# Performance work log

Hardware: AMD Instinct MI355X
Metric: run time of the kernel (lower is better)

The kernel has to match this reference:

```python
import jax, jax.numpy as jnp
import numpy as np

B = 65536
CH = 12          # chans
L = 63           # length
FBAND = 14
ZDIM = 2
FLEN = 7         # adaptive filter taps
PAD = 3          # (FLEN-1)//2
VLEN = L - FLEN + 1   # 57, 'same'-conv then crop == valid conv
FG_H = 35
EN1, EN2 = 16, 32
KW, ST = 6, 3
EN_OUT = EN2 * 5      # 160
DE_H = ZDIM * 5       # 10
DE_OUT = 50
BN_EPS = 1e-5


def setup_inputs() -> dict:
    key = jax.random.key(0)
    ks = jax.random.split(key, 24)
    f32 = jnp.float32

    def rn(k, shape, scale=0.1):
        return jax.random.normal(k, shape, f32) * scale

    return {
        "raw_eeg": jax.random.normal(ks[0], (B, CH, L), f32),
        "eegf": jax.random.normal(ks[1], (B, CH * FBAND), f32),
        "eps": jax.random.normal(ks[2], (B, ZDIM), f32),
        # filter generator: Linear(168->35), Tanh, Linear(35->7), Tanh
        "fg_w1": rn(ks[3], (FG_H, CH * FBAND)), "fg_b1": rn(ks[4], (FG_H,)),
        "fg_w2": rn(ks[5], (FLEN, FG_H)), "fg_b2": rn(ks[6], (FLEN,)),
        # encoder convs + batchnorms
        "enc_w1": rn(ks[7], (EN1, CH, KW)), "enc_b1": rn(ks[8], (EN1,)),
        "bn1_g": jnp.ones((EN1,), f32), "bn1_b": jnp.zeros((EN1,), f32),
        "enc_w2": rn(ks[9], (EN2, EN1, KW)), "enc_b2": rn(ks[10], (EN2,)),
        "bn2_g": jnp.ones((EN2,), f32), "bn2_b": jnp.zeros((EN2,), f32),
        # latent heads
        "mu_w": rn(ks[11], (ZDIM, EN_OUT)), "mu_b": rn(ks[12], (ZDIM,)),
        "lv_w": rn(ks[13], (ZDIM, EN_OUT)), "lv_b": rn(ks[14], (ZDIM,)),
        # decoder: Linear(2->10), Tanh, Linear(10->50), Tanh
        "de_w1": rn(ks[15], (DE_H, ZDIM)), "de_b1": rn(ks[16], (DE_H,)),
        "de_w2": rn(ks[17], (DE_OUT, DE_H)), "de_b2": rn(ks[18], (DE_OUT,)),
    }


def _linear(x, w, b):
    return x @ w.T + b


def _batchnorm(x, g, b):
    # torch BatchNorm1d, training mode: biased variance over (N, L) per channel
    mean = jnp.mean(x, axis=(0, 2), keepdims=True)
    var = jnp.mean(jnp.square(x - mean), axis=(0, 2), keepdims=True)
    xn = (x - mean) * jax.lax.rsqrt(var + BN_EPS)
    return xn * g[None, :, None] + b[None, :, None]


def _conv1d(x, w, b, stride):
    y = jax.lax.conv_general_dilated(
        x, w, window_strides=(stride,), padding="VALID",
        dimension_numbers=("NCH", "OIH", "NCH"))
    return y + b[None, :, None]


def reference(raw_eeg, eegf, eps,
              fg_w1, fg_b1, fg_w2, fg_b2,
              enc_w1, enc_b1, bn1_g, bn1_b,
              enc_w2, enc_b2, bn2_g, bn2_b,
              mu_w, mu_b, lv_w, lv_b,
              de_w1, de_b1, de_w2, de_b2):
    bsz = raw_eeg.shape[0]
    # per-sample 7-tap adaptive filter  [B, FLEN]
    filt = jnp.tanh(_linear(jnp.tanh(_linear(eegf, fg_w1, fg_b1)), fg_w2, fg_b2))
    # per-sample depthwise cross-correlation, 'same' conv then pad:-pad crop
    # == VALID correlation: eeg[b,c,t] = sum_k raw[b,c,t+k] * filt[b,k]
    eeg = sum(raw_eeg[:, :, k:k + VLEN] * filt[:, None, k, None]
              for k in range(FLEN))                      # [B, CH, 57]
    # encoder
    h = jnp.tanh(_batchnorm(_conv1d(eeg, enc_w1, enc_b1, ST), bn1_g, bn1_b))   # [B,16,18]
    h = jnp.tanh(_batchnorm(_conv1d(h, enc_w2, enc_b2, ST), bn2_g, bn2_b))     # [B,32,5]
    h = h.reshape(bsz, -1)                                # [B,160]
    mu = _linear(h, mu_w, mu_b)                           # [B,2]
    logvar = _linear(h, lv_w, lv_b)                       # [B,2]
    z = mu + eps * jnp.exp(0.5 * logvar)                  # reparameterize
    d = jnp.tanh(_linear(z, de_w1, de_b1))
    output = jnp.tanh(_linear(d, de_w2, de_b2))           # [B,50]
    return (output, mu, logvar)
```

## Files before the change

### kernel.cpp

```cpp
#include <hip/hip_runtime.h>
#include <hip/hip_bf16.h>

#define BATCH   65536
#define NCHAN   12
#define LRAW    63
#define CHF     168
#define FLEN    7
#define VLEN    57
#define FGH     35
#define EN1     16
#define EN2     32
#define KWID    6
#define LC1     18
#define LC2     5

#define SH1     64
#define SH2     32

static const size_t WS_STATS1 = 0;
static const size_t WS_STATS2 = 2048;
static const size_t WS_COEF   = 4096;
static const size_t WS_W1T    = 4192;
static const size_t WS_W2T    = WS_W1T + 1152;
static const size_t WS_FILT   = WS_W2T + 3072;
static const size_t WS_C1     = WS_FILT + (size_t)BATCH * 8;

__global__ void k_init(const float* __restrict__ ew1, const float* __restrict__ ew2,
                       float* __restrict__ w1t, float* __restrict__ w2t,
                       float* __restrict__ stats) {
    int t = threadIdx.x;
    for (int i = t; i < 4096; i += 256) stats[i] = 0.f;
    for (int i = t; i < EN1 * NCHAN * KWID; i += 256) {
        int oc = i / (NCHAN * KWID); int r = i % (NCHAN * KWID);
        w1t[r * EN1 + oc] = ew1[i];
    }
    for (int i = t; i < EN2 * EN1 * KWID; i += 256) {
        int oc = i / (EN1 * KWID); int r = i % (EN1 * KWID);
        w2t[r * EN2 + oc] = ew2[i];
    }
}

__global__ __launch_bounds__(256) void k_fg(
        const float* __restrict__ eegf,
        const float* __restrict__ w1, const float* __restrict__ b1,
        const float* __restrict__ w2, const float* __restrict__ b2,
        float* __restrict__ filt) {
    int b = blockIdx.x * 256 + threadIdx.x;
    const float* xr = eegf + (size_t)b * CHF;
    float acc[FGH];
#pragma unroll
    for (int j = 0; j < FGH; j++) acc[j] = b1[j];
#pragma unroll 1
    for (int t0 = 0; t0 < CHF; t0 += 56) {
        float x[56];
#pragma unroll
        for (int q = 0; q < 14; q++) {
            float4 v = *reinterpret_cast<const float4*>(xr + t0 + 4 * q);
            x[4*q] = v.x; x[4*q+1] = v.y; x[4*q+2] = v.z; x[4*q+3] = v.w;
        }
#pragma unroll 1
        for (int j = 0; j < FGH; j++) {
            const float* wr = w1 + (size_t)j * CHF + t0;
            float s0 = 0.f, s1 = 0.f, s2 = 0.f, s3 = 0.f;
#pragma unroll
            for (int q = 0; q < 14; q++) {
                s0 = fmaf(x[4*q],   wr[4*q],   s0);
                s1 = fmaf(x[4*q+1], wr[4*q+1], s1);
                s2 = fmaf(x[4*q+2], wr[4*q+2], s2);
                s3 = fmaf(x[4*q+3], wr[4*q+3], s3);
            }
            acc[j] += (s0 + s1) + (s2 + s3);
        }
    }
    float fa[FLEN];
#pragma unroll
    for (int k = 0; k < FLEN; k++) fa[k] = b2[k];
#pragma unroll 1
    for (int j = 0; j < FGH; j++) {
        float h = tanhf(acc[j]);
#pragma unroll
        for (int k = 0; k < FLEN; k++) fa[k] = fmaf(h, w2[k * FGH + j], fa[k]);
    }
    float4 o0, o1;
    o0.x = tanhf(fa[0]); o0.y = tanhf(fa[1]); o0.z = tanhf(fa[2]); o0.w = tanhf(fa[3]);
    o1.x = tanhf(fa[4]); o1.y = tanhf(fa[5]); o1.z = tanhf(fa[6]); o1.w = 0.f;
    float4* fo = reinterpret_cast<float4*>(filt + (size_t)b * 8);
    fo[0] = o0; fo[1] = o1;
}

__global__ __launch_bounds__(320) void k_conv1(
        const float* __restrict__ raw, const float* __restrict__ encb1,
        const float* __restrict__ filtbuf, const float* __restrict__ w1t,
        float* __restrict__ c1, float* __restrict__ stats1) {
    __shared__ float4 rawt4[3024];
    __shared__ float filts[16][9];
    float* rawt = (float*)rawt4;
    const int tid = threadIdx.x;
    const int s0b = blockIdx.x * 16;
    const float4* src4 = reinterpret_cast<const float4*>(raw + (size_t)s0b * 756);
#pragma unroll
    for (int k = 0; k < 10; k++) {
        int idx = tid + k * 320;
        if (idx < 3024) rawt4[idx] = src4[idx];
    }
    if (tid < 112) {
        int s = tid / 7, k = tid % 7;
        filts[s][k] = filtbuf[(size_t)(s0b + s) * 8 + k];
    }
    __syncthreads();
    const int s = tid & 15;
    const int pg = tid >> 4;
    float acc[EN1];
#pragma unroll
    for (int o = 0; o < EN1; o++) acc[o] = encb1[o];
    if (pg < 18) {
        const float f0 = filts[s][0], f1 = filts[s][1], f2 = filts[s][2], f3 = filts[s][3],
                    f4 = filts[s][4], f5 = filts[s][5], f6 = filts[s][6];
        const float* rbase = rawt + s * 756 + 3 * pg;
#pragma unroll 1
        for (int c = 0; c < NCHAN; c++) {
            const float* rp = rbase + c * 63;
            float rv[12];
#pragma unroll
            for (int j = 0; j < 12; j++) rv[j] = rp[j];
            float e[KWID];
#pragma unroll
            for (int j = 0; j < KWID; j++) {
                float v = f0 * rv[j];
                v = fmaf(f1, rv[j+1], v);
                v = fmaf(f2, rv[j+2], v);
                v = fmaf(f3, rv[j+3], v);
                v = fmaf(f4, rv[j+4], v);
                v = fmaf(f5, rv[j+5], v);
                v = fmaf(f6, rv[j+6], v);
                e[j] = v;
            }
            const float* wp = w1t + c * (KWID * EN1);
#pragma unroll
            for (int j = 0; j < KWID; j++)
#pragma unroll
                for (int o = 0; o < EN1; o++)
                    acc[o] = fmaf(e[j], wp[j * EN1 + o], acc[o]);
        }
    }
    __syncthreads();
    float* c1t = rawt;
    if (pg < 18) {
#pragma unroll
        for (int o = 0; o < EN1; o++) c1t[s * 305 + o * 19 + pg] = acc[o];
    }
    __syncthreads();
    float* c1g = c1 + (size_t)s0b * 288;
#pragma unroll 1
    for (int ss = 0; ss < 16; ss++) {
        if (tid < 288) {
            int oc = tid / 18, p = tid - oc * 18;
            c1g[ss * 288 + tid] = c1t[ss * 305 + oc * 19 + p];
        }
    }
    if (tid < 256) {
        const int oc = tid >> 4, g = tid & 15;
        float sm = 0.f, sq = 0.f;
#pragma unroll
        for (int p = 0; p < 18; p++) {
            float v = c1t[g * 305 + oc * 19 + p];
            sm += v; sq = fmaf(v, v, sq);
        }
#pragma unroll
        for (int m = 8; m >= 1; m >>= 1) {
            sm += __shfl_xor(sm, m);
            sq += __shfl_xor(sq, m);
        }
        if (g == 0) {
            float* base = stats1 + (blockIdx.x & (SH1 - 1)) * 32;
            atomicAdd(base + oc, sm);
            atomicAdd(base + 16 + oc, sq);
        }
    }
}

__global__ void k_bnfin(const float* __restrict__ g, const float* __restrict__ bb,
                        const float* __restrict__ shards, int nsh, int nch,
                        float* __restrict__ ca, float* __restrict__ cb,
                        float invn) {
    int t = threadIdx.x;
    if (t < nch) {
        float sm = 0.f, sq = 0.f;
        for (int i = 0; i < nsh; i++) {
            sm += shards[i * 2 * nch + t];
            sq += shards[i * 2 * nch + nch + t];
        }
        float mean = sm * invn;
        float var  = sq * invn - mean * mean;
        float a = g[t] * rsqrtf(var + 1e-5f);
        ca[t] = a;
        cb[t] = bb[t] - mean * a;
    }
}

__global__ __launch_bounds__(256) void k_conv2(
        const float* __restrict__ encb2, const float* __restrict__ bn1c,
        const float* __restrict__ w2t, float* __restrict__ c1,
        float* __restrict__ stats2) {
    __shared__ float e1s[32 * 289];
    const int tid = threadIdx.x;
    const int s0b = blockIdx.x * 32;
    float* c1g = c1 + (size_t)s0b * 288;
    const int sl = tid >> 3, g = tid & 7;
    {
        const float4* row4 = reinterpret_cast<const float4*>(c1g + sl * 288);
#pragma unroll 1
        for (int kk = 0; kk < 9; kk++) {
            int fo = kk * 8 + g;
            float4 v = row4[fo];
            float r[4] = {v.x, v.y, v.z, v.w};
            int i0 = fo * 4;
#pragma unroll
            for (int u = 0; u < 4; u++) {
                int i = i0 + u;
                int ch = i / 18;
                e1s[sl * 289 + i] = tanhf(fmaf(r[u], bn1c[ch], bn1c[16 + ch]));
            }
        }
    }
    __syncthreads();
    const int s = tid & 31, p = tid >> 5;
    float acc[EN2];
#pragma unroll
    for (int o = 0; o < EN2; o++) acc[o] = encb2[o];
    if (p < 5) {
        const float* eS = e1s + s * 289;
#pragma unroll 1
        for (int c = 0; c < EN1; c++) {
#pragma unroll
            for (int j = 0; j < KWID; j++) {
                float ev = eS[c * 18 + 3 * p + j];
                const float* wp = w2t + (c * KWID + j) * EN2;
#pragma unroll
                for (int o = 0; o < EN2; o++) acc[o] = fmaf(ev, wp[o], acc[o]);
            }
        }
    }
    __syncthreads();
    float* c2t = e1s;
    if (p < 5) {
#pragma unroll
        for (int o = 0; o < EN2; o++) c2t[s * 161 + o * 5 + p] = acc[o];
    }
    __syncthreads();
    {
        float4* row4 = reinterpret_cast<float4*>(c1g + sl * 288);
#pragma unroll 1
        for (int kk = 0; kk < 5; kk++) {
            int fo = kk * 8 + g;
            int i0 = fo * 4;
            float4 w;
            w.x = c2t[sl * 161 + i0];
            w.y = c2t[sl * 161 + i0 + 1];
            w.z = c2t[sl * 161 + i0 + 2];
            w.w = c2t[sl * 161 + i0 + 3];
            row4[fo] = w;
        }
    }
    {
        const int oc = tid >> 3, g8 = tid & 7;
        float sm = 0.f, sq = 0.f;
#pragma unroll 1
        for (int mm = 0; mm < 4; mm++) {
            int ss = g8 + 8 * mm;
#pragma unroll
            for (int pp = 0; pp < 5; pp++) {
                float v = c2t[ss * 161 + oc * 5 + pp];
                sm += v; sq = fmaf(v, v, sq);
            }
        }
#pragma unroll
        for (int m = 4; m >= 1; m >>= 1) {
            sm += __shfl_xor(sm, m);
            sq += __shfl_xor(sq, m);
        }
        if (g8 == 0) {
            float* base = stats2 + (blockIdx.x & (SH2 - 1)) * 64;
            atomicAdd(base + oc, sm);
            atomicAdd(base + 32 + oc, sq);
        }
    }
}

__global__ __launch_bounds__(256) void k_head(
        const float* __restrict__ eps,
        const float* __restrict__ muw, const float* __restrict__ mub,
        const float* __restrict__ lvw, const float* __restrict__ lvb,
        const float* __restrict__ dw1, const float* __restrict__ db1,
        const float* __restrict__ dw2, const float* __restrict__ db2,
        const float* __restrict__ c2, const float* __restrict__ bn2c,
        float* __restrict__ out) {
    int gid = blockIdx.x * 256 + threadIdx.x;
    int b = gid >> 2, q = gid & 3;
    const float4* c2v = reinterpret_cast<const float4*>(c2 + (size_t)b * 288 + q * 40);
    float m0 = 0.f, m1 = 0.f, l0 = 0.f, l1 = 0.f;
#pragma unroll 1
    for (int t = 0; t < 10; t++) {
        float4 v = c2v[t];
        float r[4] = {v.x, v.y, v.z, v.w};
#pragma unroll
        for (int u = 0; u < 4; u++) {
            int idx = q * 40 + t * 4 + u;
            int ch = idx / 5;
            float h = tanhf(fmaf(r[u], bn2c[ch], bn2c[32 + ch]));
            m0 = fmaf(h, muw[idx],       m0);
            m1 = fmaf(h, muw[160 + idx], m1);
            l0 = fmaf(h, lvw[idx],       l0);
            l1 = fmaf(h, lvw[160 + idx], l1);
        }
    }
#pragma unroll
    for (int m = 1; m <= 2; m <<= 1) {
        m0 += __shfl_xor(m0, m); m1 += __shfl_xor(m1, m);
        l0 += __shfl_xor(l0, m); l1 += __shfl_xor(l1, m);
    }
    m0 += mub[0]; m1 += mub[1]; l0 += lvb[0]; l1 += lvb[1];
    float2 ev = *reinterpret_cast<const float2*>(eps + (size_t)b * 2);
    float z0 = fmaf(ev.x, expf(0.5f * l0), m0);
    float z1 = fmaf(ev.y, expf(0.5f * l1), m1);
    float d[10];
#pragma unroll
    for (int j = 0; j < 10; j++)
        d[j] = tanhf(fmaf(z1, dw1[j * 2 + 1], fmaf(z0, dw1[j * 2], db1[j])));
    float* orow = out + (size_t)b * 50;
    int nkk = (q == 3) ? 7 : 6;
#pragma unroll 1
    for (int kk = 0; kk < nkk; kk++) {
        int o = (q * 6 + kk) * 2;
        float s0 = db2[o], s1 = db2[o + 1];
#pragma unroll
        for (int j = 0; j < 10; j++) {
            s0 = fmaf(d[j], dw2[o * 10 + j],       s0);
            s1 = fmaf(d[j], dw2[(o + 1) * 10 + j], s1);
        }
        float2 w; w.x = tanhf(s0); w.y = tanhf(s1);
        *reinterpret_cast<float2*>(orow + o) = w;
    }
    if (q == 0)
        *reinterpret_cast<float2*>(out + (size_t)BATCH * 50 + (size_t)b * 2) = make_float2(m0, m1);
    if (q == 1)
        *reinterpret_cast<float2*>(out + (size_t)BATCH * 52 + (size_t)b * 2) = make_float2(l0, l1);
}

extern "C" void kernel_launch(void* const* d_in, const int* in_sizes, int n_in,
                              void* d_out, int out_size, void* d_ws, size_t ws_size,
                              hipStream_t stream) {
    (void)in_sizes; (void)n_in; (void)out_size; (void)ws_size;
    const float* raw  = (const float*)d_in[0];
    const float* eegf = (const float*)d_in[1];
    const float* eps  = (const float*)d_in[2];
    const float* fgw1 = (const float*)d_in[3];
    const float* fgb1 = (const float*)d_in[4];
    const float* fgw2 = (const float*)d_in[5];
    const float* fgb2 = (const float*)d_in[6];
    const float* ew1  = (const float*)d_in[7];
    const float* eb1  = (const float*)d_in[8];
    const float* bn1g = (const float*)d_in[9];
    const float* bn1b = (const float*)d_in[10];
    const float* ew2  = (const float*)d_in[11];
    const float* eb2  = (const float*)d_in[12];
    const float* bn2g = (const float*)d_in[13];
    const float* bn2b = (const float*)d_in[14];
    const float* muw  = (const float*)d_in[15];
    const float* mub  = (const float*)d_in[16];
    const float* lvw  = (const float*)d_in[17];
    const float* lvb  = (const float*)d_in[18];
    const float* dw1  = (const float*)d_in[19];
    const float* db1  = (const float*)d_in[20];
    const float* dw2  = (const float*)d_in[21];
    const float* db2  = (const float*)d_in[22];

    float* ws     = (float*)d_ws;
    float* stats1 = ws + WS_STATS1;
    float* stats2 = ws + WS_STATS2;
    float* coef   = ws + WS_COEF;
    float* w1t    = ws + WS_W1T;
    float* w2t    = ws + WS_W2T;
    float* filt   = ws + WS_FILT;
    float* c1     = ws + WS_C1;
    float* out    = (float*)d_out;

    hipLaunchKernelGGL(k_init, dim3(1), dim3(256), 0, stream, ew1, ew2, w1t, w2t, stats1);
    hipLaunchKernelGGL(k_fg, dim3(256), dim3(256), 0, stream, eegf, fgw1, fgb1, fgw2, fgb2, filt);
    hipLaunchKernelGGL(k_conv1, dim3(4096), dim3(320), 0, stream, raw, eb1, filt, w1t, c1, stats1);
    hipLaunchKernelGGL(k_bnfin, dim3(1), dim3(64), 0, stream,
                       bn1g, bn1b, stats1, SH1, 16, coef, coef + 16,
                       1.0f / ((float)BATCH * (float)LC1));
    hipLaunchKernelGGL(k_conv2, dim3(2048), dim3(256), 0, stream, eb2, coef, w2t, c1, stats2);
    hipLaunchKernelGGL(k_bnfin, dim3(1), dim3(64), 0, stream,
                       bn2g, bn2b, stats2, SH2, 32, coef + 32, coef + 64,
                       1.0f / ((float)BATCH * (float)LC2));
    hipLaunchKernelGGL(k_head, dim3(1024), dim3(256), 0, stream,
                       eps, muw, mub, lvw, lvb, dw1, db1, dw2, db2, c1, coef + 32, out);
}
```

Measured before the change: 629.9 us.

## Store conv intermediates as bf16, fuse BN finalize, fast tanh, double-buffer conv1

```diff
diff --git a/kernel.cpp b/kernel.cpp
--- a/kernel.cpp
+++ b/kernel.cpp
@@ -6,7 +6,6 @@
 #define LRAW    63
 #define CHF     168
 #define FLEN    7
-#define VLEN    57
 #define FGH     35
 #define EN1     16
 #define EN2     32
@@ -19,11 +18,23 @@
 
 static const size_t WS_STATS1 = 0;
 static const size_t WS_STATS2 = 2048;
-static const size_t WS_COEF   = 4096;
-static const size_t WS_W1T    = 4192;
+static const size_t WS_W1T    = 4096;
 static const size_t WS_W2T    = WS_W1T + 1152;
 static const size_t WS_FILT   = WS_W2T + 3072;
 static const size_t WS_C1     = WS_FILT + (size_t)BATCH * 8;
+static const size_t WS_C2     = WS_C1 + (size_t)18 * BATCH * 16 / 2;
+
+__device__ __forceinline__ float ftanh(float x) {
+    float e = __expf(2.0f * x);
+    return fmaf(-2.0f, __builtin_amdgcn_rcpf(e + 1.0f), 1.0f);
+}
+__device__ __forceinline__ unsigned int bfr(float x) {
+    unsigned int u = __float_as_uint(x);
+    return (u + 0x7fffu + ((u >> 16) & 1u)) >> 16;
+}
+__device__ __forceinline__ float bf2f(unsigned int us) {
+    return __uint_as_float(us << 16);
+}
 
 __global__ void k_init(const float* __restrict__ ew1, const float* __restrict__ ew2,
                        float* __restrict__ w1t, float* __restrict__ w2t,
@@ -58,7 +69,7 @@
             float4 v = *reinterpret_cast<const float4*>(xr + t0 + 4 * q);
             x[4*q] = v.x; x[4*q+1] = v.y; x[4*q+2] = v.z; x[4*q+3] = v.w;
         }
-#pragma unroll 1
+#pragma unroll 5
         for (int j = 0; j < FGH; j++) {
             const float* wr = w1 + (size_t)j * CHF + t0;
             float s0 = 0.f, s1 = 0.f, s2 = 0.f, s3 = 0.f;
@@ -77,13 +88,13 @@
     for (int k = 0; k < FLEN; k++) fa[k] = b2[k];
 #pragma unroll 1
     for (int j = 0; j < FGH; j++) {
-        float h = tanhf(acc[j]);
+        float h = ftanh(acc[j]);
 #pragma unroll
         for (int k = 0; k < FLEN; k++) fa[k] = fmaf(h, w2[k * FGH + j], fa[k]);
     }
     float4 o0, o1;
-    o0.x = tanhf(fa[0]); o0.y = tanhf(fa[1]); o0.z = tanhf(fa[2]); o0.w = tanhf(fa[3]);
-    o1.x = tanhf(fa[4]); o1.y = tanhf(fa[5]); o1.z = tanhf(fa[6]); o1.w = 0.f;
+    o0.x = ftanh(fa[0]); o0.y = ftanh(fa[1]); o0.z = ftanh(fa[2]); o0.w = ftanh(fa[3]);
+    o1.x = ftanh(fa[4]); o1.y = ftanh(fa[5]); o1.z = ftanh(fa[6]); o1.w = 0.f;
     float4* fo = reinterpret_cast<float4*>(filt + (size_t)b * 8);
     fo[0] = o0; fo[1] = o1;
 }
@@ -91,144 +102,166 @@
 __global__ __launch_bounds__(320) void k_conv1(
         const float* __restrict__ raw, const float* __restrict__ encb1,
         const float* __restrict__ filtbuf, const float* __restrict__ w1t,
-        float* __restrict__ c1, float* __restrict__ stats1) {
+        unsigned short* __restrict__ c1, float* __restrict__ stats1) {
     __shared__ float4 rawt4[3024];
-    __shared__ float filts[16][9];
+    __shared__ float filts[2][16][8];
+    __shared__ float part[5][32];
     float* rawt = (float*)rawt4;
     const int tid = threadIdx.x;
-    const int s0b = blockIdx.x * 16;
+    const int s0b = blockIdx.x * 32;
     const float4* src4 = reinterpret_cast<const float4*>(raw + (size_t)s0b * 756);
 #pragma unroll
     for (int k = 0; k < 10; k++) {
         int idx = tid + k * 320;
         if (idx < 3024) rawt4[idx] = src4[idx];
     }
-    if (tid < 112) {
-        int s = tid / 7, k = tid % 7;
-        filts[s][k] = filtbuf[(size_t)(s0b + s) * 8 + k];
+    if (tid < 256) {
+        int tl = tid >> 7, r = tid & 127, s = r >> 3, k = r & 7;
+        filts[tl][s][k] = filtbuf[(size_t)(s0b + tl * 16 + s) * 8 + k];
     }
     __syncthreads();
+    float4 rr[10];
+#pragma unroll
+    for (int k = 0; k < 10; k++) {
+        int idx = tid + k * 320;
+        if (idx < 3024) rr[k] = src4[3024 + idx];
+    }
     const int s = tid & 15;
     const int pg = tid >> 4;
-    float acc[EN1];
-#pragma unroll
-    for (int o = 0; o < EN1; o++) acc[o] = encb1[o];
-    if (pg < 18) {
-        const float f0 = filts[s][0], f1 = filts[s][1], f2 = filts[s][2], f3 = filts[s][3],
-                    f4 = filts[s][4], f5 = filts[s][5], f6 = filts[s][6];
-        const float* rbase = rawt + s * 756 + 3 * pg;
-#pragma unroll 1
-        for (int c = 0; c < NCHAN; c++) {
-            const float* rp = rbase + c * 63;
-            float rv[12];
-#pragma unroll
-            for (int j = 0; j < 12; j++) rv[j] = rp[j];
-            float e[KWID];
-#pragma unroll
-            for (int j = 0; j < KWID; j++) {
-                float v = f0 * rv[j];
-                v = fmaf(f1, rv[j+1], v);
-                v = fmaf(f2, rv[j+2], v);
-                v = fmaf(f3, rv[j+3], v);
-                v = fmaf(f4, rv[j+4], v);
-                v = fmaf(f5, rv[j+5], v);
-                v = fmaf(f6, rv[j+6], v);
-                e[j] = v;
-            }
-            const float* wp = w1t + c * (KWID * EN1);
-#pragma unroll
-            for (int j = 0; j < KWID; j++)
-#pragma unroll
-                for (int o = 0; o < EN1; o++)
-                    acc[o] = fmaf(e[j], wp[j * EN1 + o], acc[o]);
-        }
-    }
-    __syncthreads();
-    float* c1t = rawt;
-    if (pg < 18) {
-#pragma unroll
-        for (int o = 0; o < EN1; o++) c1t[s * 305 + o * 19 + pg] = acc[o];
-    }
-    __syncthreads();
-    float* c1g = c1 + (size_t)s0b * 288;
-#pragma unroll 1
-    for (int ss = 0; ss < 16; ss++) {
-        if (tid < 288) {
-            int oc = tid / 18, p = tid - oc * 18;
-            c1g[ss * 288 + tid] = c1t[ss * 305 + oc * 19 + p];
-        }
-    }
-    if (tid < 256) {
-        const int oc = tid >> 4, g = tid & 15;
-        float sm = 0.f, sq = 0.f;
-#pragma unroll
-        for (int p = 0; p < 18; p++) {
-            float v = c1t[g * 305 + oc * 19 + p];
-            sm += v; sq = fmaf(v, v, sq);
-        }
-#pragma unroll
-        for (int m = 8; m >= 1; m >>= 1) {
-            sm += __shfl_xor(sm, m);
-            sq += __shfl_xor(sq, m);
-        }
-        if (g == 0) {
-            float* base = stats1 + (blockIdx.x & (SH1 - 1)) * 32;
-            atomicAdd(base + oc, sm);
-            atomicAdd(base + 16 + oc, sq);
-        }
-    }
-}
-
-__global__ void k_bnfin(const float* __restrict__ g, const float* __restrict__ bb,
-                        const float* __restrict__ shards, int nsh, int nch,
-                        float* __restrict__ ca, float* __restrict__ cb,
-                        float invn) {
-    int t = threadIdx.x;
-    if (t < nch) {
-        float sm = 0.f, sq = 0.f;
-        for (int i = 0; i < nsh; i++) {
-            sm += shards[i * 2 * nch + t];
-            sq += shards[i * 2 * nch + nch + t];
-        }
-        float mean = sm * invn;
-        float var  = sq * invn - mean * mean;
-        float a = g[t] * rsqrtf(var + 1e-5f);
-        ca[t] = a;
-        cb[t] = bb[t] - mean * a;
+    const int wv = tid >> 6;
+#pragma unroll 1
+    for (int tl = 0; tl < 2; tl++) {
+        float acc[EN1];
+        if (pg < 18) {
+#pragma unroll
+            for (int o = 0; o < EN1; o++) acc[o] = encb1[o];
+            const float f0 = filts[tl][s][0], f1 = filts[tl][s][1], f2 = filts[tl][s][2],
+                        f3 = filts[tl][s][3], f4 = filts[tl][s][4], f5 = filts[tl][s][5],
+                        f6 = filts[tl][s][6];
+            const float* rbase = rawt + s * 756 + 3 * pg;
+#pragma unroll 1
+            for (int c = 0; c < NCHAN; c++) {
+                const float* rp = rbase + c * 63;
+                float rv[12];
+#pragma unroll
+                for (int j = 0; j < 12; j++) rv[j] = rp[j];
+                float e[KWID];
+#pragma unroll
+                for (int j = 0; j < KWID; j++) {
+                    float v = f0 * rv[j];
+                    v = fmaf(f1, rv[j+1], v);
+                    v = fmaf(f2, rv[j+2], v);
+                    v = fmaf(f3, rv[j+3], v);
+                    v = fmaf(f4, rv[j+4], v);
+                    v = fmaf(f5, rv[j+5], v);
+                    v = fmaf(f6, rv[j+6], v);
+                    e[j] = v;
+                }
+                const float* wp = w1t + c * (KWID * EN1);
+#pragma unroll
+                for (int j = 0; j < KWID; j++)
+#pragma unroll
+                    for (int o = 0; o < EN1; o++)
+                        acc[o] = fmaf(e[j], wp[j * EN1 + o], acc[o]);
+            }
+            unsigned int w[8];
+#pragma unroll
+            for (int o = 0; o < 8; o++)
+                w[o] = bfr(acc[2*o]) | (bfr(acc[2*o+1]) << 16);
+            size_t base = ((size_t)pg * BATCH + (size_t)(s0b + tl*16 + s)) * 16;
+            uint4* dst = reinterpret_cast<uint4*>(c1 + base);
+            dst[0] = make_uint4(w[0], w[1], w[2], w[3]);
+            dst[1] = make_uint4(w[4], w[5], w[6], w[7]);
+        } else {
+#pragma unroll
+            for (int o = 0; o < EN1; o++) acc[o] = 0.f;
+        }
+        float sq[EN1];
+#pragma unroll
+        for (int o = 0; o < EN1; o++) sq[o] = acc[o] * acc[o];
+#pragma unroll
+        for (int m = 1; m < 64; m <<= 1) {
+#pragma unroll
+            for (int o = 0; o < EN1; o++) {
+                acc[o] += __shfl_xor(acc[o], m);
+                sq[o]  += __shfl_xor(sq[o], m);
+            }
+        }
+        if ((tid & 63) == 0) {
+#pragma unroll
+            for (int o = 0; o < EN1; o++) {
+                part[wv][o]      = acc[o];
+                part[wv][16 + o] = sq[o];
+            }
+        }
+        __syncthreads();
+        if (tid < 32) {
+            float v = part[0][tid] + part[1][tid] + part[2][tid] + part[3][tid] + part[4][tid];
+            atomicAdd(stats1 + (blockIdx.x & (SH1 - 1)) * 32 + tid, v);
+        }
+        if (tl == 0) {
+#pragma unroll
+            for (int k = 0; k < 10; k++) {
+                int idx = tid + k * 320;
+                if (idx < 3024) rawt4[idx] = rr[k];
+            }
+            __syncthreads();
+        }
     }
 }
 
 __global__ __launch_bounds__(256) void k_conv2(
-        const float* __restrict__ encb2, const float* __restrict__ bn1c,
-        const float* __restrict__ w2t, float* __restrict__ c1,
+        const float* __restrict__ encb2,
+        const float* __restrict__ bn1g, const float* __restrict__ bn1b,
+        const float* __restrict__ stats1, const float* __restrict__ w2t,
+        const unsigned short* __restrict__ c1, unsigned short* __restrict__ c2,
         float* __restrict__ stats2) {
     __shared__ float e1s[32 * 289];
+    __shared__ float bn1c[32];
+    __shared__ float part[4][64];
     const int tid = threadIdx.x;
     const int s0b = blockIdx.x * 32;
-    float* c1g = c1 + (size_t)s0b * 288;
-    const int sl = tid >> 3, g = tid & 7;
-    {
-        const float4* row4 = reinterpret_cast<const float4*>(c1g + sl * 288);
-#pragma unroll 1
-        for (int kk = 0; kk < 9; kk++) {
-            int fo = kk * 8 + g;
-            float4 v = row4[fo];
-            float r[4] = {v.x, v.y, v.z, v.w};
-            int i0 = fo * 4;
+    if (tid < 16) {
+        float sm = 0.f, sqr = 0.f;
+#pragma unroll 8
+        for (int i = 0; i < SH1; i++) {
+            sm  += stats1[i * 32 + tid];
+            sqr += stats1[i * 32 + 16 + tid];
+        }
+        const float invn = 1.0f / ((float)BATCH * (float)LC1);
+        float mean = sm * invn;
+        float var  = sqr * invn - mean * mean;
+        float a = bn1g[tid] * rsqrtf(var + 1e-5f);
+        bn1c[tid] = a;
+        bn1c[16 + tid] = bn1b[tid] - mean * a;
+    }
+    __syncthreads();
+    const uint4* c1u = reinterpret_cast<const uint4*>(c1);
+#pragma unroll
+    for (int k = 0; k < 5; k++) {
+        int idx = tid + k * 256;
+        if (idx < 1152) {
+            int p = idx >> 6, rem = idx & 63, ss = rem >> 1, half = rem & 1;
+            uint4 v = c1u[((size_t)p * BATCH + (s0b + ss)) * 2 + half];
+            unsigned int ww[4] = {v.x, v.y, v.z, v.w};
+            float* eb = e1s + ss * 289 + p;
 #pragma unroll
             for (int u = 0; u < 4; u++) {
-                int i = i0 + u;
-                int ch = i / 18;
-                e1s[sl * 289 + i] = tanhf(fmaf(r[u], bn1c[ch], bn1c[16 + ch]));
+                int oc0 = half * 8 + 2 * u;
+                float f0 = bf2f(ww[u] & 0xffffu);
+                float f1 = __uint_as_float(ww[u] & 0xffff0000u);
+                eb[oc0 * 18]       = ftanh(fmaf(f0, bn1c[oc0],     bn1c[16 + oc0]));
+                eb[(oc0 + 1) * 18] = ftanh(fmaf(f1, bn1c[oc0 + 1], bn1c[16 + oc0 + 1]));
             }
         }
     }
     __syncthreads();
     const int s = tid & 31, p = tid >> 5;
+    const bool act = (p < 5);
     float acc[EN2];
-#pragma unroll
-    for (int o = 0; o < EN2; o++) acc[o] = encb2[o];
-    if (p < 5) {
+    if (act) {
+#pragma unroll
+        for (int o = 0; o < EN2; o++) acc[o] = encb2[o];
         const float* eS = e1s + s * 289;
 #pragma unroll 1
         for (int c = 0; c < EN1; c++) {
@@ -240,50 +273,37 @@
                 for (int o = 0; o < EN2; o++) acc[o] = fmaf(ev, wp[o], acc[o]);
             }
         }
+#pragma unroll
+        for (int o = 0; o < EN2; o++)
+            c2[(size_t)(o * 5 + p) * BATCH + (s0b + s)] = (unsigned short)bfr(acc[o]);
+    } else {
+#pragma unroll
+        for (int o = 0; o < EN2; o++) acc[o] = 0.f;
+    }
+    float sq[EN2];
+#pragma unroll
+    for (int o = 0; o < EN2; o++) sq[o] = acc[o] * acc[o];
+#pragma unroll
+    for (int m = 1; m < 64; m <<= 1) {
+#pragma unroll
+        for (int o = 0; o < EN2; o++) {
+            acc[o] += __shfl_xor(acc[o], m);
+            sq[o]  += __shfl_xor(sq[o], m);
+        }
+    }
+    const int lane = tid & 63, wv = tid >> 6;
+    if (lane == 0) {
+#pragma unroll
+        for (int o = 0; o < EN2; o++) part[wv][o] = acc[o];
+    }
+    if (lane == 1) {
+#pragma unroll
+        for (int o = 0; o < EN2; o++) part[wv][32 + o] = sq[o];
     }
     __syncthreads();
-    float* c2t = e1s;
-    if (p < 5) {
-#pragma unroll
-        for (int o = 0; o < EN2; o++) c2t[s * 161 + o * 5 + p] = acc[o];
-    }
-    __syncthreads();
-    {
-        float4* row4 = reinterpret_cast<float4*>(c1g + sl * 288);
-#pragma unroll 1
-        for (int kk = 0; kk < 5; kk++) {
-            int fo = kk * 8 + g;
-            int i0 = fo * 4;
-            float4 w;
-            w.x = c2t[sl * 161 + i0];
-            w.y = c2t[sl * 161 + i0 + 1];
-            w.z = c2t[sl * 161 + i0 + 2];
-            w.w = c2t[sl * 161 + i0 + 3];
-            row4[fo] = w;
-        }
-    }
-    {
-        const int oc = tid >> 3, g8 = tid & 7;
-        float sm = 0.f, sq = 0.f;
-#pragma unroll 1
-        for (int mm = 0; mm < 4; mm++) {
-            int ss = g8 + 8 * mm;
-#pragma unroll
-            for (int pp = 0; pp < 5; pp++) {
-                float v = c2t[ss * 161 + oc * 5 + pp];
-                sm += v; sq = fmaf(v, v, sq);
-            }
-        }
-#pragma unroll
-        for (int m = 4; m >= 1; m >>= 1) {
-            sm += __shfl_xor(sm, m);
-            sq += __shfl_xor(sq, m);
-        }
-        if (g8 == 0) {
-            float* base = stats2 + (blockIdx.x & (SH2 - 1)) * 64;
-            atomicAdd(base + oc, sm);
-            atomicAdd(base + 32 + oc, sq);
-        }
+    if (tid < 64) {
+        float v = part[0][tid] + part[1][tid] + part[2][tid] + part[3][tid];
+        atomicAdd(stats2 + (blockIdx.x & (SH2 - 1)) * 64 + tid, v);
     }
 }
 
@@ -293,26 +313,40 @@
         const float* __restrict__ lvw, const float* __restrict__ lvb,
         const float* __restrict__ dw1, const float* __restrict__ db1,
         const float* __restrict__ dw2, const float* __restrict__ db2,
-        const float* __restrict__ c2, const float* __restrict__ bn2c,
+        const unsigned short* __restrict__ c2, const float* __restrict__ stats2,
+        const float* __restrict__ bn2g, const float* __restrict__ bn2b,
         float* __restrict__ out) {
-    int gid = blockIdx.x * 256 + threadIdx.x;
+    __shared__ float bn2c[64];
+    const int tid = threadIdx.x;
+    if (tid < 32) {
+        float sm = 0.f, sqr = 0.f;
+#pragma unroll 8
+        for (int i = 0; i < SH2; i++) {
+            sm  += stats2[i * 64 + tid];
+            sqr += stats2[i * 64 + 32 + tid];
+        }
+        const float invn = 1.0f / ((float)BATCH * (float)LC2);
+        float mean = sm * invn;
+        float var  = sqr * invn - mean * mean;
+        float a = bn2g[tid] * rsqrtf(var + 1e-5f);
+        bn2c[tid] = a;
+        bn2c[32 + tid] = bn2b[tid] - mean * a;
+    }
+    __syncthreads();
+    int gid = blockIdx.x * 256 + tid;
     int b = gid >> 2, q = gid & 3;
-    const float4* c2v = reinterpret_cast<const float4*>(c2 + (size_t)b * 288 + q * 40);
+    const unsigned short* cp = c2 + (size_t)q * 40 * BATCH + b;
     float m0 = 0.f, m1 = 0.f, l0 = 0.f, l1 = 0.f;
-#pragma unroll 1
-    for (int t = 0; t < 10; t++) {
-        float4 v = c2v[t];
-        float r[4] = {v.x, v.y, v.z, v.w};
-#pragma unroll
-        for (int u = 0; u < 4; u++) {
-            int idx = q * 40 + t * 4 + u;
-            int ch = idx / 5;
-            float h = tanhf(fmaf(r[u], bn2c[ch], bn2c[32 + ch]));
-            m0 = fmaf(h, muw[idx],       m0);
-            m1 = fmaf(h, muw[160 + idx], m1);
-            l0 = fmaf(h, lvw[idx],       l0);
-            l1 = fmaf(h, lvw[160 + idx], l1);
-        }
+#pragma unroll
+    for (int t = 0; t < 40; t++) {
+        int idx = q * 40 + t;
+        int ch = q * 8 + (t / 5);
+        float x = bf2f((unsigned int)cp[(size_t)t * BATCH]);
+        float h = ftanh(fmaf(x, bn2c[ch], bn2c[32 + ch]));
+        m0 = fmaf(h, muw[idx],       m0);
+        m1 = fmaf(h, muw[160 + idx], m1);
+        l0 = fmaf(h, lvw[idx],       l0);
+        l1 = fmaf(h, lvw[160 + idx], l1);
     }
 #pragma unroll
     for (int m = 1; m <= 2; m <<= 1) {
@@ -321,12 +355,12 @@
     }
     m0 += mub[0]; m1 += mub[1]; l0 += lvb[0]; l1 += lvb[1];
     float2 ev = *reinterpret_cast<const float2*>(eps + (size_t)b * 2);
-    float z0 = fmaf(ev.x, expf(0.5f * l0), m0);
-    float z1 = fmaf(ev.y, expf(0.5f * l1), m1);
+    float z0 = fmaf(ev.x, __expf(0.5f * l0), m0);
+    float z1 = fmaf(ev.y, __expf(0.5f * l1), m1);
     float d[10];
 #pragma unroll
     for (int j = 0; j < 10; j++)
-        d[j] = tanhf(fmaf(z1, dw1[j * 2 + 1], fmaf(z0, dw1[j * 2], db1[j])));
+        d[j] = ftanh(fmaf(z1, dw1[j * 2 + 1], fmaf(z0, dw1[j * 2], db1[j])));
     float* orow = out + (size_t)b * 50;
     int nkk = (q == 3) ? 7 : 6;
 #pragma unroll 1
@@ -338,7 +372,7 @@
             s0 = fmaf(d[j], dw2[o * 10 + j],       s0);
             s1 = fmaf(d[j], dw2[(o + 1) * 10 + j], s1);
         }
-        float2 w; w.x = tanhf(s0); w.y = tanhf(s1);
+        float2 w; w.x = ftanh(s0); w.y = ftanh(s1);
         *reinterpret_cast<float2*>(orow + o) = w;
     }
     if (q == 0)
@@ -378,23 +412,21 @@
     float* ws     = (float*)d_ws;
     float* stats1 = ws + WS_STATS1;
     float* stats2 = ws + WS_STATS2;
-    float* coef   = ws + WS_COEF;
     float* w1t    = ws + WS_W1T;
     float* w2t    = ws + WS_W2T;
     float* filt   = ws + WS_FILT;
-    float* c1     = ws + WS_C1;
+    unsigned short* c1 = (unsigned short*)(ws + WS_C1);
+    unsigned short* c2 = (unsigned short*)(ws + WS_C2);
     float* out    = (float*)d_out;
 
     hipLaunchKernelGGL(k_init, dim3(1), dim3(256), 0, stream, ew1, ew2, w1t, w2t, stats1);
-    hipLaunchKernelGGL(k_fg, dim3(256), dim3(256), 0, stream, eegf, fgw1, fgb1, fgw2, fgb2, filt);
-    hipLaunchKernelGGL(k_conv1, dim3(4096), dim3(320), 0, stream, raw, eb1, filt, w1t, c1, stats1);
-    hipLaunchKernelGGL(k_bnfin, dim3(1), dim3(64), 0, stream,
-                       bn1g, bn1b, stats1, SH1, 16, coef, coef + 16,
-                       1.0f / ((float)BATCH * (float)LC1));
-    hipLaunchKernelGGL(k_conv2, dim3(2048), dim3(256), 0, stream, eb2, coef, w2t, c1, stats2);
-    hipLaunchKernelGGL(k_bnfin, dim3(1), dim3(64), 0, stream,
-                       bn2g, bn2b, stats2, SH2, 32, coef + 32, coef + 64,
-                       1.0f / ((float)BATCH * (float)LC2));
+    hipLaunchKernelGGL(k_fg, dim3(256), dim3(256), 0, stream,
+                       eegf, fgw1, fgb1, fgw2, fgb2, filt);
+    hipLaunchKernelGGL(k_conv1, dim3(2048), dim3(320), 0, stream,
+                       raw, eb1, filt, w1t, c1, stats1);
+    hipLaunchKernelGGL(k_conv2, dim3(2048), dim3(256), 0, stream,
+                       eb2, bn1g, bn1b, stats1, w2t, c1, c2, stats2);
     hipLaunchKernelGGL(k_head, dim3(1024), dim3(256), 0, stream,
-                       eps, muw, mub, lvw, lvb, dw1, db1, dw2, db2, c1, coef + 32, out);
-}
+                       eps, muw, mub, lvw, lvb, dw1, db1, dw2, db2,
+                       c2, stats2, bn2g, bn2b, out);
+}
```

After: 648.2 us. 1.03x slower.
